# Kernel tuning notes

Hardware: AMD Instinct MI355X
Metric: run time of the kernel (lower is better)

## Reference

```python
import jax, jax.numpy as jnp
import numpy as np

DIM = 512
NUM_HEADS = 8
HEAD_DIM = DIM // NUM_HEADS
SCALE = HEAD_DIM ** -0.5


def setup_inputs() -> dict:
    key = jax.random.key(0)
    k1, k2, k3, k4 = jax.random.split(key, 4)
    x = jax.random.normal(k1, (2, 4096, DIM), dtype=jnp.float32)
    # Linear weights stored as (in, out) for x @ W; torch Linear(dim, 3*dim, bias=False)
    w_qkv = jax.random.normal(k2, (DIM, 3 * DIM), dtype=jnp.float32) * (DIM ** -0.5)
    w_proj = jax.random.normal(k3, (DIM, DIM), dtype=jnp.float32) * (DIM ** -0.5)
    b_proj = jax.random.normal(k4, (DIM,), dtype=jnp.float32) * 0.02
    return {"x": x, "w_qkv": w_qkv, "w_proj": w_proj, "b_proj": b_proj}


def reference(x, w_qkv, w_proj, b_proj):
    B, N, C = x.shape
    qkv = (x @ w_qkv).reshape(B, N, 3, NUM_HEADS, HEAD_DIM)
    qkv = jnp.transpose(qkv, (2, 0, 3, 1, 4))  # (3, B, H, N, hd)
    q, k, v = qkv[0], qkv[1], qkv[2]
    attn = jnp.einsum("bhnd,bhmd->bhnm", q, k) * SCALE
    attn = jax.nn.softmax(attn, axis=-1)
    out = jnp.einsum("bhnm,bhmd->bhnd", attn, v)
    out = jnp.transpose(out, (0, 2, 1, 3)).reshape(B, N, C)
    return out @ w_proj + b_proj
```

## Files before the change

### kernel.cpp

```cpp
#include <hip/hip_runtime.h>
#include <hip/hip_bf16.h>
#include <stdint.h>
#include <math.h>

#define NC3 1536
#define QSCALE 0.18033688011111907f

typedef __attribute__((ext_vector_type(8))) short short8;
typedef __attribute__((ext_vector_type(4))) short short4v;
typedef __attribute__((ext_vector_type(4))) float f32x4;
typedef __attribute__((ext_vector_type(16))) float f32x16;

static __device__ __forceinline__ short f2bf(float f) {
    union { __hip_bfloat16 h; short s; } u;
    u.h = __float2bfloat16(f);
    return u.s;
}
static __device__ __forceinline__ unsigned bfpack(float a, float b) {
    unsigned ua = (__float_as_uint(a) + 0x8000u) >> 16;
    unsigned ub = (__float_as_uint(b) + 0x8000u) & 0xffff0000u;
    return ua | ub;
}

#define GLD_LDS(g, l)                                                          \
    __builtin_amdgcn_global_load_lds(                                          \
        (const __attribute__((address_space(1))) void*)(g),                    \
        (__attribute__((address_space(3))) void*)(l), 16, 0, 0)

__global__ __launch_bounds__(256) void cast_f32_bf16(const float* __restrict__ src,
                                                     short* __restrict__ dst, int n4) {
    int i = blockIdx.x * 256 + threadIdx.x;
    if (i < n4) {
        float4 v = ((const float4*)src)[i];
        short4v o = {f2bf(v.x), f2bf(v.y), f2bf(v.z), f2bf(v.w)};
        ((short4v*)dst)[i] = o;
    }
}

__global__ __launch_bounds__(256) void transpose_f32_bf16(const float* __restrict__ src,
                                                          short* __restrict__ dst,
                                                          int R, int C) {
    __shared__ short t[32][33];
    int c0 = blockIdx.x * 32, r0 = blockIdx.y * 32;
    int tx = threadIdx.x, ty = threadIdx.y;
#pragma unroll
    for (int i = 0; i < 4; i++)
        t[ty + i * 8][tx] = f2bf(src[(size_t)(r0 + ty + i * 8) * C + c0 + tx]);
    __syncthreads();
#pragma unroll
    for (int i = 0; i < 4; i++)
        dst[(size_t)(c0 + ty + i * 8) * R + r0 + tx] = t[tx][ty + i * 8];
}

__global__ __launch_bounds__(256) void transpose_v(const short* __restrict__ QKV,
                                                   short* __restrict__ VT) {
    __shared__ short t[32][33];
    int n0 = blockIdx.x * 32, d0 = blockIdx.y * 32;
    int bh = blockIdx.z;
    int b = bh >> 3, h = bh & 7;
    const short* src = QKV + (size_t)b * 4096 * NC3 + 1024 + h * 64;
    short* dst = VT + (size_t)bh * 64 * 4096;
    int tx = threadIdx.x, ty = threadIdx.y;
#pragma unroll
    for (int i = 0; i < 4; i++)
        t[ty + i * 8][tx] = src[(size_t)(n0 + ty + i * 8) * NC3 + d0 + tx];
    __syncthreads();
#pragma unroll
    for (int i = 0; i < 4; i++)
        dst[(size_t)(d0 + ty + i * 8) * 4096 + n0 + tx] = t[tx][ty + i * 8];
}

template <int NMODE>
__global__ __launch_bounds__(256) void gemm128(const short* __restrict__ A,
                                               const short* __restrict__ Bt,
                                               short* __restrict__ OutB,
                                               float* __restrict__ OutF,
                                               const float* __restrict__ bias) {
    __shared__ __attribute__((aligned(16))) short a_sm[128 * 64];
    __shared__ __attribute__((aligned(16))) short b_sm[128 * 64];
    const int tid = threadIdx.x;
    const int lane = tid & 63;
    const int wave = tid >> 6;
    const int wr = wave >> 1, wc = wave & 1;
    const int quad = lane >> 4;
    const int l15 = lane & 15;
    const int m0 = blockIdx.x * 128;
    const int n0 = blockIdx.y * 128;
    const int srow = lane >> 3;
    const int schunk = (lane & 7) ^ srow;

    f32x4 zero4 = {0.f, 0.f, 0.f, 0.f};
    f32x4 acc[4][4];
#pragma unroll
    for (int i = 0; i < 4; i++)
#pragma unroll
        for (int j = 0; j < 4; j++) acc[i][j] = zero4;

    for (int k0 = 0; k0 < 512; k0 += 64) {
        __syncthreads();
#pragma unroll
        for (int i = 0; i < 4; i++) {
            int r0 = wave * 32 + i * 8;
            const short* ga = A + (size_t)(m0 + r0 + srow) * 512 + k0 + schunk * 8;
            GLD_LDS(ga, a_sm + r0 * 64);
            const short* gb = Bt + (size_t)(n0 + r0 + srow) * 512 + k0 + schunk * 8;
            GLD_LDS(gb, b_sm + r0 * 64);
        }
        __syncthreads();
#pragma unroll
        for (int kk = 0; kk < 2; kk++) {
            short8 af[4], bfr[4];
#pragma unroll
            for (int mi = 0; mi < 4; mi++) {
                int row = wr * 64 + mi * 16 + l15;
                int slot = (kk * 4 + quad) ^ (row & 7);
                af[mi] = *(const short8*)(a_sm + row * 64 + slot * 8);
            }
#pragma unroll
            for (int ni = 0; ni < 4; ni++) {
                int row = wc * 64 + ni * 16 + l15;
                int slot = (kk * 4 + quad) ^ (row & 7);
                bfr[ni] = *(const short8*)(b_sm + row * 64 + slot * 8);
            }
#pragma unroll
            for (int mi = 0; mi < 4; mi++)
#pragma unroll
                for (int ni = 0; ni < 4; ni++)
                    acc[mi][ni] = __builtin_amdgcn_mfma_f32_16x16x32_bf16(
                        af[mi], bfr[ni], acc[mi][ni], 0, 0, 0);
        }
    }

#pragma unroll
    for (int mi = 0; mi < 4; mi++) {
#pragma unroll
        for (int ni = 0; ni < 4; ni++) {
            int gm0 = m0 + wr * 64 + mi * 16 + quad * 4;
            int gn = n0 + wc * 64 + ni * 16 + l15;
            f32x4 v = acc[mi][ni];
#pragma unroll
            for (int r = 0; r < 4; r++) {
                int gm = gm0 + r;
                float val = v[r];
                if (NMODE == 0) {
                    float o = (gn < 512) ? val * QSCALE : val;
                    OutB[(size_t)gm * NC3 + gn] = f2bf(o);
                } else {
                    OutF[(size_t)gm * 512 + gn] = val + bias[gn];
                }
            }
        }
    }
}

__global__ __launch_bounds__(256, 2) void attn_kernel(const short* __restrict__ QKV,
                                                      const short* __restrict__ VT,
                                                      short* __restrict__ AO) {
    __shared__ __attribute__((aligned(16))) short k_sm[2][64 * 64];
    __shared__ __attribute__((aligned(16))) short v_sm[2][64 * 64];

    const int tid = threadIdx.x;
    const int lane = tid & 63;
    const int wave = tid >> 6;
    const int l31 = lane & 31;
    const int hi = lane >> 5;
    const int qt = blockIdx.x;
    const int bh = blockIdx.y;
    const int b = bh >> 3, h = bh & 7;
    const size_t tokbase = (size_t)b * 4096;
    const int rowbase = qt * 128;
    const short* Qg = QKV + h * 64;
    const short* Kg = QKV + 512 + h * 64;
    const short* VTg = VT + (size_t)bh * 64 * 4096;
    const int srow = lane >> 3;
    const int schunk = (lane & 7) ^ srow;

    short* qstage = &k_sm[0][0];
#pragma unroll
    for (int i = 0; i < 4; i++) {
        int r0 = wave * 32 + i * 8;
        GLD_LDS(Qg + (tokbase + rowbase + r0 + srow) * NC3 + schunk * 8, qstage + r0 * 64);
    }
    __syncthreads();
    const int qrow = wave * 32 + l31;
    short8 qf[4];
#pragma unroll
    for (int kk = 0; kk < 4; kk++) {
        int slot = (kk * 2 + hi) ^ (qrow & 7);
        qf[kk] = *(const short8*)(qstage + qrow * 64 + slot * 8);
    }
    __syncthreads();

#pragma unroll
    for (int i = 0; i < 2; i++) {
        int r0 = wave * 16 + i * 8;
        GLD_LDS(Kg + (tokbase + r0 + srow) * NC3 + schunk * 8, k_sm[0] + r0 * 64);
        GLD_LDS(VTg + (size_t)(r0 + srow) * 4096 + schunk * 8, v_sm[0] + r0 * 64);
    }

    const short onebf = (short)0x3F80;
    const short8 ones = {onebf, onebf, onebf, onebf, onebf, onebf, onebf, onebf};

    f32x16 acc_o[2], acc_l;
#pragma unroll
    for (int i = 0; i < 16; i++) { acc_o[0][i] = 0.f; acc_o[1][i] = 0.f; acc_l[i] = 0.f; }

    for (int kt = 0; kt < 64; kt++) {
        __syncthreads();
        const int cur = kt & 1;
        if (kt < 63) {
            const int nb = cur ^ 1;
#pragma unroll
            for (int i = 0; i < 2; i++) {
                int r0 = wave * 16 + i * 8;
                GLD_LDS(Kg + (tokbase + (size_t)(kt + 1) * 64 + r0 + srow) * NC3 + schunk * 8,
                        k_sm[nb] + r0 * 64);
                GLD_LDS(VTg + (size_t)(r0 + srow) * 4096 + (kt + 1) * 64 + schunk * 8,
                        v_sm[nb] + r0 * 64);
            }
        }

        f32x16 s[2];
#pragma unroll
        for (int i = 0; i < 16; i++) { s[0][i] = 0.f; s[1][i] = 0.f; }
#pragma unroll
        for (int kk = 0; kk < 4; kk++) {
#pragma unroll
            for (int kb = 0; kb < 2; kb++) {
                int row = kb * 32 + l31;
                int slot = (kk * 2 + hi) ^ (row & 7);
                short8 kf = *(const short8*)(k_sm[cur] + row * 64 + slot * 8);
                s[kb] = __builtin_amdgcn_mfma_f32_32x32x16_bf16(kf, qf[kk], s[kb], 0, 0, 0);
            }
        }

        unsigned pk[2][8];
#pragma unroll
        for (int kb = 0; kb < 2; kb++)
#pragma unroll
            for (int i = 0; i < 16; i += 2)
                pk[kb][i >> 1] = bfpack(__builtin_amdgcn_exp2f(s[kb][i]),
                                        __builtin_amdgcn_exp2f(s[kb][i + 1]));

        short8 pf[4];
#pragma unroll
        for (int kb = 0; kb < 2; kb++) {
#pragma unroll
            for (int f = 0; f < 2; f++) {
                unsigned b0 = pk[kb][4 * f + 0], b1 = pk[kb][4 * f + 1];
                unsigned b2 = pk[kb][4 * f + 2], b3 = pk[kb][4 * f + 3];
                unsigned s0 = hi ? b0 : b2;
                unsigned s1 = hi ? b1 : b3;
                unsigned t0 = (unsigned)__shfl_xor((int)s0, 32, 64);
                unsigned t1 = (unsigned)__shfl_xor((int)s1, 32, 64);
                union { unsigned u[4]; short8 s8; } cv;
                cv.u[0] = hi ? t0 : b0;
                cv.u[1] = hi ? t1 : b1;
                cv.u[2] = hi ? b2 : t0;
                cv.u[3] = hi ? b3 : t1;
                pf[kb * 2 + f] = cv.s8;
            }
        }

#pragma unroll
        for (int g = 0; g < 4; g++) {
            acc_l = __builtin_amdgcn_mfma_f32_32x32x16_bf16(ones, pf[g], acc_l, 0, 0, 0);
#pragma unroll
            for (int db = 0; db < 2; db++) {
                int row = db * 32 + l31;
                int slot = (g * 2 + hi) ^ (row & 7);
                short8 vf = *(const short8*)(v_sm[cur] + row * 64 + slot * 8);
                acc_o[db] = __builtin_amdgcn_mfma_f32_32x32x16_bf16(vf, pf[g], acc_o[db], 0, 0, 0);
            }
        }
    }

    __syncthreads();

    float inv = 1.0f / acc_l[0];
    short* osm = &k_sm[0][0] + wave * 2048;
#pragma unroll
    for (int db = 0; db < 2; db++) {
#pragma unroll
        for (int i = 0; i < 16; i += 2) {
            int d = db * 32 + (i & 3) + 8 * (i >> 2) + 4 * hi;
            unsigned pkd = bfpack(acc_o[db][i] * inv, acc_o[db][i + 1] * inv);
            int slot = (d >> 3) ^ (l31 & 7);
            *(unsigned*)(osm + l31 * 64 + slot * 8 + (d & 7)) = pkd;
        }
    }
#pragma unroll
    for (int j = 0; j < 4; j++) {
        int r = lane >> 1;
        int c = (lane & 1) * 4 + j;
        int slot = c ^ (r & 7);
        short8 ov = *(const short8*)(osm + r * 64 + slot * 8);
        size_t grow = tokbase + rowbase + wave * 32 + r;
        *(short8*)(AO + grow * 512 + h * 64 + c * 8) = ov;
    }
}

extern "C" void kernel_launch(void* const* d_in, const int* in_sizes, int n_in,
                              void* d_out, int out_size, void* d_ws, size_t ws_size,
                              hipStream_t stream) {
    (void)in_sizes; (void)n_in; (void)out_size; (void)ws_size;
    const float* x = (const float*)d_in[0];
    const float* wqkv = (const float*)d_in[1];
    const float* wproj = (const float*)d_in[2];
    const float* bproj = (const float*)d_in[3];
    float* out = (float*)d_out;

    short* ws = (short*)d_ws;
    short* xbf = ws;
    short* wqkvT = xbf + (size_t)4194304;
    short* wprojT = wqkvT + (size_t)1536 * 512;
    short* QKV = wprojT + (size_t)512 * 512;
    short* VTb = QKV + (size_t)8192 * 1536;
    short* AO = VTb + (size_t)16 * 64 * 4096;

    cast_f32_bf16<<<4096, 256, 0, stream>>>(x, xbf, 1048576);
    transpose_f32_bf16<<<dim3(48, 16), dim3(32, 8), 0, stream>>>(wqkv, wqkvT, 512, 1536);
    transpose_f32_bf16<<<dim3(16, 16), dim3(32, 8), 0, stream>>>(wproj, wprojT, 512, 512);
    gemm128<0><<<dim3(64, 12), 256, 0, stream>>>(xbf, wqkvT, QKV, nullptr, nullptr);
    transpose_v<<<dim3(128, 2, 16), dim3(32, 8), 0, stream>>>(QKV, VTb);
    attn_kernel<<<dim3(32, 16), 256, 0, stream>>>(QKV, VTb, AO);
    gemm128<1><<<dim3(64, 4), 256, 0, stream>>>(AO, wprojT, nullptr, out, bproj);
}
```

Baseline: 225.8 us.

## Split attention over the key dimension into two partials and add a combine kernel

The attention kernel gains a third grid dimension that splits the 64 key tiles into two halves. Each half writes unnormalized bf16 output partials and its row sums to scratch buffers, reusing the xbf and wqkvT workspace that is dead by then. A new combine kernel adds the two partials and divides by the summed denominators. This doubles the block count, and launch bounds are raised to allow four blocks per CU, to improve occupancy and latency hiding. The cost is an extra launch, additional global traffic, bf16 rounding of the unnormalized partials, and possible register pressure from the tighter bound.

```diff
diff --git a/kernel.cpp b/kernel.cpp
--- a/kernel.cpp
+++ b/kernel.cpp
@@ -5,6 +5,7 @@
 
 #define NC3 1536
 #define QSCALE 0.18033688011111907f
+#define KSPLIT 2
 
 typedef __attribute__((ext_vector_type(8))) short short8;
 typedef __attribute__((ext_vector_type(4))) short short4v;
@@ -15,6 +16,9 @@
     union { __hip_bfloat16 h; short s; } u;
     u.h = __float2bfloat16(f);
     return u.s;
+}
+static __device__ __forceinline__ float bf2f(short s) {
+    return __uint_as_float(((unsigned)(unsigned short)s) << 16);
 }
 static __device__ __forceinline__ unsigned bfpack(float a, float b) {
     unsigned ua = (__float_as_uint(a) + 0x8000u) >> 16;
@@ -68,6 +72,23 @@
 #pragma unroll
     for (int i = 0; i < 4; i++)
         dst[(size_t)(d0 + ty + i * 8) * 4096 + n0 + tx] = t[tx][ty + i * 8];
+}
+
+__global__ __launch_bounds__(256) void combine_partials(const short* __restrict__ Op0,
+                                                        const short* __restrict__ Op1,
+                                                        const float* __restrict__ lp,
+                                                        short* __restrict__ AO) {
+    int i = (blockIdx.x * 256 + threadIdx.x) * 8;
+    int row = i >> 9;
+    int h = (i >> 6) & 7;
+    float linv = 1.0f / (lp[row * 8 + h] + lp[65536 + row * 8 + h]);
+    short8 a = *(const short8*)(Op0 + i);
+    short8 b = *(const short8*)(Op1 + i);
+    short8 o;
+#pragma unroll
+    for (int j = 0; j < 8; j++)
+        o[j] = f2bf((bf2f(a[j]) + bf2f(b[j])) * linv);
+    *(short8*)(AO + i) = o;
 }
 
 template <int NMODE>
@@ -153,9 +174,11 @@
     }
 }
 
-__global__ __launch_bounds__(256, 2) void attn_kernel(const short* __restrict__ QKV,
+__global__ __launch_bounds__(256, 4) void attn_kernel(const short* __restrict__ QKV,
                                                       const short* __restrict__ VT,
-                                                      short* __restrict__ AO) {
+                                                      short* __restrict__ Op0,
+                                                      short* __restrict__ Op1,
+                                                      float* __restrict__ lpart) {
     __shared__ __attribute__((aligned(16))) short k_sm[2][64 * 64];
     __shared__ __attribute__((aligned(16))) short v_sm[2][64 * 64];
 
@@ -166,9 +189,12 @@
     const int hi = lane >> 5;
     const int qt = blockIdx.x;
     const int bh = blockIdx.y;
+    const int ks = blockIdx.z;
     const int b = bh >> 3, h = bh & 7;
     const size_t tokbase = (size_t)b * 4096;
     const int rowbase = qt * 128;
+    const int kt0 = ks * (64 / KSPLIT);
+    const int kt1 = kt0 + (64 / KSPLIT);
     const short* Qg = QKV + h * 64;
     const short* Kg = QKV + 512 + h * 64;
     const short* VTg = VT + (size_t)bh * 64 * 4096;
@@ -194,8 +220,10 @@
 #pragma unroll
     for (int i = 0; i < 2; i++) {
         int r0 = wave * 16 + i * 8;
-        GLD_LDS(Kg + (tokbase + r0 + srow) * NC3 + schunk * 8, k_sm[0] + r0 * 64);
-        GLD_LDS(VTg + (size_t)(r0 + srow) * 4096 + schunk * 8, v_sm[0] + r0 * 64);
+        GLD_LDS(Kg + (tokbase + (size_t)kt0 * 64 + r0 + srow) * NC3 + schunk * 8,
+                k_sm[0] + r0 * 64);
+        GLD_LDS(VTg + (size_t)(r0 + srow) * 4096 + kt0 * 64 + schunk * 8,
+                v_sm[0] + r0 * 64);
     }
 
     const short onebf = (short)0x3F80;
@@ -205,10 +233,10 @@
 #pragma unroll
     for (int i = 0; i < 16; i++) { acc_o[0][i] = 0.f; acc_o[1][i] = 0.f; acc_l[i] = 0.f; }
 
-    for (int kt = 0; kt < 64; kt++) {
+    for (int kt = kt0; kt < kt1; kt++) {
         __syncthreads();
         const int cur = kt & 1;
-        if (kt < 63) {
+        if (kt < kt1 - 1) {
             const int nb = cur ^ 1;
 #pragma unroll
             for (int i = 0; i < 2; i++) {
@@ -277,18 +305,21 @@
 
     __syncthreads();
 
-    float inv = 1.0f / acc_l[0];
+    size_t growq = tokbase + rowbase + qrow;
+    if (hi == 0) lpart[(size_t)ks * 65536 + growq * 8 + h] = acc_l[0];
+
     short* osm = &k_sm[0][0] + wave * 2048;
 #pragma unroll
     for (int db = 0; db < 2; db++) {
 #pragma unroll
         for (int i = 0; i < 16; i += 2) {
             int d = db * 32 + (i & 3) + 8 * (i >> 2) + 4 * hi;
-            unsigned pkd = bfpack(acc_o[db][i] * inv, acc_o[db][i + 1] * inv);
+            unsigned pkd = bfpack(acc_o[db][i], acc_o[db][i + 1]);
             int slot = (d >> 3) ^ (l31 & 7);
             *(unsigned*)(osm + l31 * 64 + slot * 8 + (d & 7)) = pkd;
         }
     }
+    short* Od = (ks == 0) ? Op0 : Op1;
 #pragma unroll
     for (int j = 0; j < 4; j++) {
         int r = lane >> 1;
@@ -296,7 +327,7 @@
         int slot = c ^ (r & 7);
         short8 ov = *(const short8*)(osm + r * 64 + slot * 8);
         size_t grow = tokbase + rowbase + wave * 32 + r;
-        *(short8*)(AO + grow * 512 + h * 64 + c * 8) = ov;
+        *(short8*)(Od + grow * 512 + h * 64 + c * 8) = ov;
     }
 }
 
@@ -317,12 +348,15 @@
     short* QKV = wprojT + (size_t)512 * 512;
     short* VTb = QKV + (size_t)8192 * 1536;
     short* AO = VTb + (size_t)16 * 64 * 4096;
+    short* Opart1 = xbf;
+    float* lpart = (float*)wqkvT;
 
     cast_f32_bf16<<<4096, 256, 0, stream>>>(x, xbf, 1048576);
     transpose_f32_bf16<<<dim3(48, 16), dim3(32, 8), 0, stream>>>(wqkv, wqkvT, 512, 1536);
     transpose_f32_bf16<<<dim3(16, 16), dim3(32, 8), 0, stream>>>(wproj, wprojT, 512, 512);
     gemm128<0><<<dim3(64, 12), 256, 0, stream>>>(xbf, wqkvT, QKV, nullptr, nullptr);
     transpose_v<<<dim3(128, 2, 16), dim3(32, 8), 0, stream>>>(QKV, VTb);
-    attn_kernel<<<dim3(32, 16), 256, 0, stream>>>(QKV, VTb, AO);
+    attn_kernel<<<dim3(32, 16, KSPLIT), 256, 0, stream>>>(QKV, VTb, AO, Opart1, lpart);
+    combine_partials<<<2048, 256, 0, stream>>>(AO, Opart1, lpart, AO);
     gemm128<1><<<dim3(64, 4), 256, 0, stream>>>(AO, wprojT, nullptr, out, bproj);
 }
```

Result: faster. 219.8 us (-2.6%).
